# Performance work log

Hardware: AMD Instinct MI355X
Metric: run time of the kernel (lower is better)

Reference implementation:

```python
import jax, jax.numpy as jnp
import numpy as np

N, E, IN_DIM, HID, OUT = 50000, 800000, 128, 128, 64


def setup_inputs() -> dict:
    key = jax.random.key(0)
    k = jax.random.split(key, 6)
    h = jax.random.normal(k[0], (N, IN_DIM), dtype=jnp.float32)
    edge_index = jax.random.randint(k[1], (2, E), 0, N, dtype=jnp.int64)
    s_in, s_hid = 1.0 / np.sqrt(IN_DIM), 1.0 / np.sqrt(HID)
    W_gcn = jax.random.uniform(k[2], (IN_DIM, HID), jnp.float32, -s_in, s_in)
    b_gcn = jnp.zeros((HID,), jnp.float32)
    W_fc = jax.random.uniform(k[3], (HID, OUT), jnp.float32, -s_hid, s_hid)
    b_fc = jax.random.uniform(k[4], (OUT,), jnp.float32, -s_hid, s_hid)
    return {"h": h, "edge_index": edge_index, "W_gcn": W_gcn,
            "b_gcn": b_gcn, "W_fc": W_fc, "b_fc": b_fc}


def reference(h, edge_index, W_gcn, b_gcn, W_fc, b_fc):
    n = h.shape[0]
    # GCNConv: transform, add self-loops, symmetric normalization, scatter-add
    x = h @ W_gcn                                   # [N, HID]
    loop = jnp.arange(n, dtype=edge_index.dtype)
    row = jnp.concatenate([edge_index[0], loop])    # source nodes
    col = jnp.concatenate([edge_index[1], loop])    # destination nodes
    deg = jax.ops.segment_sum(jnp.ones_like(col, dtype=x.dtype), col,
                              num_segments=n)       # in-degree incl. self-loop
    dinv = jnp.where(deg > 0, jax.lax.rsqrt(deg), 0.0)
    norm = dinv[row] * dinv[col]                    # [E+N]
    msg = x[row] * norm[:, None]                    # gather + scale
    agg = jax.ops.segment_sum(msg, col, num_segments=n) + b_gcn
    # ReLU then projection
    return jax.nn.relu(agg) @ W_fc + b_fc
```

## Files before the change

kernel.cpp:

```cpp
#include <hip/hip_runtime.h>

#define N_NODES 50000
#define N_EDGES 800000
#define NBKT 782
#define BINB 196
#define BCAP 1792
#define UTS 136

typedef __attribute__((ext_vector_type(4))) float floatx4;
typedef __attribute__((ext_vector_type(8))) _Float16 half8;
typedef __attribute__((ext_vector_type(4))) _Float16 half4;
typedef __attribute__((ext_vector_type(2))) _Float16 half2v;

#define O_GF    0UL
#define O_W1    3200UL
#define O_W2    35968UL
#define O_STG   52480UL
#define O_H16   5657856UL

__global__ __launch_bounds__(256) void k_bin(const int* __restrict__ ei,
                                             int* __restrict__ gfill,
                                             unsigned* __restrict__ staging,
                                             const float* __restrict__ Wg,
                                             const float* __restrict__ Wf,
                                             _Float16* __restrict__ W1,
                                             _Float16* __restrict__ W2) {
    int b = blockIdx.x, t = threadIdx.x;
    if (b >= BINB) {
        int wb = b - BINB;
        if (wb < 64) {
            int i = wb * 256 + t;
            int n = i >> 7, k = i & 127;
            W1[i] = (_Float16)Wg[k * 128 + n];
        } else {
            int i = (wb - 64) * 256 + t;
            int n = i >> 7, k = i & 127;
            W2[i] = (_Float16)Wf[k * 64 + n];
        }
        return;
    }
    __shared__ int cnt[NBKT];
    __shared__ int gbase[NBKT];
    __shared__ int s_i64;
    if (t < 64) {
        unsigned w = ((const unsigned*)ei)[2 * t + 1];
        unsigned long long m = __ballot(w == 0u);
        if (t == 0) s_i64 = (__popcll(m) >= 60) ? 1 : 0;
    }
    for (int i = t; i < NBKT; i += 256) cnt[i] = 0;
    __syncthreads();
    bool i64 = s_i64 != 0;
    int e0 = b * 4096 + t * 16;
    int sv[16], dvv[16];
    if (i64) {
        const int4* ps = (const int4*)(ei) + (e0 >> 1);
        const int4* pd = (const int4*)(ei + 2 * (size_t)N_EDGES) + (e0 >> 1);
#pragma unroll
        for (int g = 0; g < 8; ++g) {
            if (e0 + 2 * g < N_EDGES) {
                int4 s4 = ps[g], d4 = pd[g];
                sv[2 * g] = s4.x; sv[2 * g + 1] = s4.z;
                dvv[2 * g] = d4.x; dvv[2 * g + 1] = d4.z;
            } else { dvv[2 * g] = -1; dvv[2 * g + 1] = -1; }
        }
    } else {
        const int4* ps = (const int4*)(ei) + (e0 >> 2);
        const int4* pd = (const int4*)(ei + (size_t)N_EDGES) + (e0 >> 2);
#pragma unroll
        for (int g = 0; g < 4; ++g) {
            if (e0 + 4 * g < N_EDGES) {
                int4 s4 = ps[g], d4 = pd[g];
                sv[4 * g] = s4.x; sv[4 * g + 1] = s4.y; sv[4 * g + 2] = s4.z; sv[4 * g + 3] = s4.w;
                dvv[4 * g] = d4.x; dvv[4 * g + 1] = d4.y; dvv[4 * g + 2] = d4.z; dvv[4 * g + 3] = d4.w;
            } else { dvv[4 * g] = -1; dvv[4 * g + 1] = -1; dvv[4 * g + 2] = -1; dvv[4 * g + 3] = -1; }
        }
    }
    unsigned pk[16]; int rk[16]; short bk[16];
#pragma unroll
    for (int j = 0; j < 16; ++j) {
        int d = dvv[j];
        if (d >= 0 && e0 + j < N_EDGES) {
            int bkt = d >> 6;
            bk[j] = (short)bkt;
            pk[j] = (unsigned)sv[j] | ((unsigned)(d & 63) << 16);
            rk[j] = atomicAdd(&cnt[bkt], 1);
        } else bk[j] = -1;
    }
    __syncthreads();
    for (int i = t; i < NBKT; i += 256)
        gbase[i] = atomicAdd(&gfill[i], cnt[i]);
    __syncthreads();
#pragma unroll
    for (int j = 0; j < 16; ++j) {
        if (bk[j] >= 0) {
            int pos = gbase[bk[j]] + rk[j];
            if (pos < BCAP) staging[(size_t)bk[j] * BCAP + pos] = pk[j];
        }
    }
}

__global__ __launch_bounds__(256) void k_conv(const float* __restrict__ h,
                                              const int* __restrict__ gfill,
                                              const unsigned* __restrict__ staging,
                                              _Float16* __restrict__ h16) {
    __shared__ int deg[128];
    __shared__ float sdv[128];
    int b = blockIdx.x, t = threadIdx.x;
    int nb = b * 128;
    int nn = min(128, N_NODES - nb);
    if (nn <= 0) return;
    if (t < 128) deg[t] = 0;
    __syncthreads();
#pragma unroll
    for (int kb = 0; kb < 2; ++kb) {
        int gb = b * 2 + kb;
        int cnt = min(gfill[gb], BCAP);
        const unsigned* st = staging + (size_t)gb * BCAP;
        for (int i = t; i < cnt; i += 256)
            atomicAdd(&deg[kb * 64 + (st[i] >> 16)], 1);
    }
    __syncthreads();
    if (t < 128) sdv[t] = rsqrtf((float)(deg[t] + 1));
    __syncthreads();
    const floatx4* src = (const floatx4*)(h + (size_t)nb * 128);
    half4* dst = (half4*)(h16 + (size_t)nb * 128);
    int nq = nn * 32;
    for (int i = t; i < nq; i += 256) {
        floatx4 v = src[i];
        float s = sdv[i >> 5];
        half4 o;
        o[0] = (_Float16)(v[0] * s); o[1] = (_Float16)(v[1] * s);
        o[2] = (_Float16)(v[2] * s); o[3] = (_Float16)(v[3] * s);
        dst[i] = o;
    }
}

__global__ __launch_bounds__(256, 8) void k_aggF(const _Float16* __restrict__ h16,
                                                 const int* __restrict__ gfill,
                                                 const unsigned* __restrict__ staging,
                                                 const _Float16* __restrict__ W1,
                                                 const _Float16* __restrict__ W2,
                                                 const float* __restrict__ bg,
                                                 const float* __restrict__ bfc,
                                                 float* __restrict__ out) {
    __shared__ _Float16 ut[16 * UTS];
    __shared__ _Float16 z[16 * UTS];
    __shared__ unsigned short se[BCAP];
    __shared__ int deg16[16], seg16[16], cur16[16];
    __shared__ float sdv16[16];
    int t = threadIdx.x;
    int wave = t >> 6;
    int lane = t & 63;
    int nb = blockIdx.x * 16;
    int bkt = blockIdx.x >> 2;
    unsigned lo = (unsigned)(blockIdx.x & 3) * 16;
    int cnt = min(gfill[bkt], BCAP);
    if (t < 16) deg16[t] = 0;
    __syncthreads();
    const unsigned* st = staging + (size_t)bkt * BCAP;
    unsigned held[7];
#pragma unroll
    for (int r = 0; r < 7; ++r) {
        int i = t + r * 256;
        unsigned p = 0xFFFFFFFFu;
        if (i < cnt) p = st[i];
        unsigned tg = p >> 16;
        if (tg - lo < 16u) atomicAdd(&deg16[tg - lo], 1);
        else p = 0xFFFFFFFFu;
        held[r] = p;
    }
    __syncthreads();
    if (t == 0) {
        int s = 0;
#pragma unroll
        for (int k = 0; k < 16; ++k) { seg16[k] = s; cur16[k] = s; s += deg16[k]; }
    }
    if (t < 16) sdv16[t] = rsqrtf((float)(deg16[t] + 1));
    __syncthreads();
#pragma unroll
    for (int r = 0; r < 7; ++r) {
        unsigned p = held[r];
        if (p != 0xFFFFFFFFu) {
            int rk = atomicAdd(&cur16[(p >> 16) - lo], 1);
            if (rk < BCAP) se[rk] = (unsigned short)(p & 0xffffu);
        }
    }
    __syncthreads();
    for (int q = 0; q < 4; ++q) {
        int tag = wave * 4 + q;
        int node = nb + tag;
        int p0 = seg16[tag];
        int p1 = p0 + deg16[tag];
        half2v us = *(const half2v*)(h16 + (size_t)node * 128 + lane * 2);
        float a0 = (float)us[0], a1 = (float)us[1];
        for (int base = p0; base < p1; base += 64) {
            int c = p1 - base; if (c > 64) c = 64;
            int idx = 0;
            if (lane < c) idx = se[base + lane];
            int j = 0;
            for (; j + 8 <= c; j += 8) {
                int s0 = __shfl(idx, j),     s1 = __shfl(idx, j + 1);
                int s2 = __shfl(idx, j + 2), s3 = __shfl(idx, j + 3);
                int s4 = __shfl(idx, j + 4), s5 = __shfl(idx, j + 5);
                int s6 = __shfl(idx, j + 6), s7 = __shfl(idx, j + 7);
                half2v u0 = *(const half2v*)(h16 + (size_t)s0 * 128 + lane * 2);
                half2v u1 = *(const half2v*)(h16 + (size_t)s1 * 128 + lane * 2);
                half2v u2 = *(const half2v*)(h16 + (size_t)s2 * 128 + lane * 2);
                half2v u3 = *(const half2v*)(h16 + (size_t)s3 * 128 + lane * 2);
                half2v u4 = *(const half2v*)(h16 + (size_t)s4 * 128 + lane * 2);
                half2v u5 = *(const half2v*)(h16 + (size_t)s5 * 128 + lane * 2);
                half2v u6 = *(const half2v*)(h16 + (size_t)s6 * 128 + lane * 2);
                half2v u7 = *(const half2v*)(h16 + (size_t)s7 * 128 + lane * 2);
                a0 += (float)u0[0] + (float)u1[0] + (float)u2[0] + (float)u3[0]
                    + (float)u4[0] + (float)u5[0] + (float)u6[0] + (float)u7[0];
                a1 += (float)u0[1] + (float)u1[1] + (float)u2[1] + (float)u3[1]
                    + (float)u4[1] + (float)u5[1] + (float)u6[1] + (float)u7[1];
            }
            for (; j + 4 <= c; j += 4) {
                int s0 = __shfl(idx, j),     s1 = __shfl(idx, j + 1);
                int s2 = __shfl(idx, j + 2), s3 = __shfl(idx, j + 3);
                half2v u0 = *(const half2v*)(h16 + (size_t)s0 * 128 + lane * 2);
                half2v u1 = *(const half2v*)(h16 + (size_t)s1 * 128 + lane * 2);
                half2v u2 = *(const half2v*)(h16 + (size_t)s2 * 128 + lane * 2);
                half2v u3 = *(const half2v*)(h16 + (size_t)s3 * 128 + lane * 2);
                a0 += (float)u0[0] + (float)u1[0] + (float)u2[0] + (float)u3[0];
                a1 += (float)u0[1] + (float)u1[1] + (float)u2[1] + (float)u3[1];
            }
            for (; j < c; ++j) {
                int s = __shfl(idx, j);
                half2v uu = *(const half2v*)(h16 + (size_t)s * 128 + lane * 2);
                a0 += (float)uu[0]; a1 += (float)uu[1];
            }
        }
        float sc = sdv16[tag];
        int r = wave * 4 + q;
        ut[r * UTS + lane * 2]     = (_Float16)(a0 * sc);
        ut[r * UTS + lane * 2 + 1] = (_Float16)(a1 * sc);
    }
    __syncthreads();
    int quad = lane >> 4, l15 = lane & 15;
    half8 a[4];
#pragma unroll
    for (int kk = 0; kk < 4; ++kk)
        a[kk] = *(const half8*)(ut + l15 * UTS + kk * 32 + quad * 8);
#pragma unroll
    for (int tt = 0; tt < 2; ++tt) {
        floatx4 acc = {0.f, 0.f, 0.f, 0.f};
        int n = (wave * 2 + tt) * 16 + l15;
#pragma unroll
        for (int kk = 0; kk < 4; ++kk) {
            half8 bb = *(const half8*)(W1 + n * 128 + kk * 32 + quad * 8);
            acc = __builtin_amdgcn_mfma_f32_16x16x32_f16(a[kk], bb, acc, 0, 0, 0);
        }
        float bias = bg[n];
#pragma unroll
        for (int i = 0; i < 4; ++i)
            z[(quad * 4 + i) * UTS + n] = (_Float16)fmaxf(acc[i] + bias, 0.f);
    }
    __syncthreads();
    half8 a2[4];
#pragma unroll
    for (int kk = 0; kk < 4; ++kk)
        a2[kk] = *(const half8*)(z + l15 * UTS + kk * 32 + quad * 8);
    {
        floatx4 acc = {0.f, 0.f, 0.f, 0.f};
        int n = wave * 16 + l15;
#pragma unroll
        for (int kk = 0; kk < 4; ++kk) {
            half8 bb = *(const half8*)(W2 + n * 128 + kk * 32 + quad * 8);
            acc = __builtin_amdgcn_mfma_f32_16x16x32_f16(a2[kk], bb, acc, 0, 0, 0);
        }
        float bias = bfc[n];
#pragma unroll
        for (int i = 0; i < 4; ++i)
            out[(size_t)(nb + quad * 4 + i) * 64 + n] = acc[i] + bias;
    }
}

extern "C" void kernel_launch(void* const* d_in, const int* in_sizes, int n_in,
                              void* d_out, int out_size, void* d_ws, size_t ws_size,
                              hipStream_t stream) {
    (void)in_sizes; (void)n_in; (void)out_size; (void)ws_size;
    const float* h  = (const float*)d_in[0];
    const int*   ei = (const int*)d_in[1];
    const float* Wg = (const float*)d_in[2];
    const float* bg = (const float*)d_in[3];
    const float* Wf = (const float*)d_in[4];
    const float* bf = (const float*)d_in[5];
    float* out = (float*)d_out;

    char* ws = (char*)d_ws;
    int*      gfill = (int*)(ws + O_GF);
    _Float16* W1    = (_Float16*)(ws + O_W1);
    _Float16* W2    = (_Float16*)(ws + O_W2);
    unsigned* staging = (unsigned*)(ws + O_STG);
    _Float16* h16   = (_Float16*)(ws + O_H16);

    hipMemsetAsync(gfill, 0, NBKT * sizeof(int), stream);
    k_bin<<<BINB + 96, 256, 0, stream>>>(ei, gfill, staging, Wg, Wf, W1, W2);
    k_conv<<<(N_NODES + 127) / 128, 256, 0, stream>>>(h, gfill, staging, h16);
    k_aggF<<<N_NODES / 16, 256, 0, stream>>>(h16, gfill, staging,
                                             W1, W2, bg, bf, out);
}
```

Baseline: 154.1 us.

## Replace block-local binning with per-edge global atomics on padded counters

The edge-binning kernel drops its shared-memory count/prefix phase and instead reserves each edge's slot with a global atomicAdd on a per-bucket counter. Each counter is padded to 64 bytes to avoid false sharing. Blocks now handle 1024 edges instead of 4096, giving more, lighter blocks and removing two block barriers. The cost is roughly 800k global atomics instead of a few per bucket per block, so contention on hot buckets may raise binning cost. Workspace offsets and the memset size grow to fit the padded counters.

```diff
diff --git a/kernel.cpp b/kernel.cpp
--- a/kernel.cpp
+++ b/kernel.cpp
@@ -3,7 +3,7 @@
 #define N_NODES 50000
 #define N_EDGES 800000
 #define NBKT 782
-#define BINB 196
+#define BINB 782
 #define BCAP 1792
 #define UTS 136
 
@@ -13,10 +13,10 @@
 typedef __attribute__((ext_vector_type(2))) _Float16 half2v;
 
 #define O_GF    0UL
-#define O_W1    3200UL
-#define O_W2    35968UL
-#define O_STG   52480UL
-#define O_H16   5657856UL
+#define O_W1    50048UL
+#define O_W2    82816UL
+#define O_STG   99200UL
+#define O_H16   5704576UL
 
 __global__ __launch_bounds__(256) void k_bin(const int* __restrict__ ei,
                                              int* __restrict__ gfill,
@@ -39,24 +39,21 @@
         }
         return;
     }
-    __shared__ int cnt[NBKT];
-    __shared__ int gbase[NBKT];
     __shared__ int s_i64;
     if (t < 64) {
         unsigned w = ((const unsigned*)ei)[2 * t + 1];
         unsigned long long m = __ballot(w == 0u);
         if (t == 0) s_i64 = (__popcll(m) >= 60) ? 1 : 0;
     }
-    for (int i = t; i < NBKT; i += 256) cnt[i] = 0;
     __syncthreads();
     bool i64 = s_i64 != 0;
-    int e0 = b * 4096 + t * 16;
-    int sv[16], dvv[16];
+    int e0 = b * 1024 + t * 4;
+    int sv[4], dvv[4];
     if (i64) {
         const int4* ps = (const int4*)(ei) + (e0 >> 1);
         const int4* pd = (const int4*)(ei + 2 * (size_t)N_EDGES) + (e0 >> 1);
 #pragma unroll
-        for (int g = 0; g < 8; ++g) {
+        for (int g = 0; g < 2; ++g) {
             if (e0 + 2 * g < N_EDGES) {
                 int4 s4 = ps[g], d4 = pd[g];
                 sv[2 * g] = s4.x; sv[2 * g + 1] = s4.z;
@@ -64,37 +61,21 @@
             } else { dvv[2 * g] = -1; dvv[2 * g + 1] = -1; }
         }
     } else {
-        const int4* ps = (const int4*)(ei) + (e0 >> 2);
-        const int4* pd = (const int4*)(ei + (size_t)N_EDGES) + (e0 >> 2);
-#pragma unroll
-        for (int g = 0; g < 4; ++g) {
-            if (e0 + 4 * g < N_EDGES) {
-                int4 s4 = ps[g], d4 = pd[g];
-                sv[4 * g] = s4.x; sv[4 * g + 1] = s4.y; sv[4 * g + 2] = s4.z; sv[4 * g + 3] = s4.w;
-                dvv[4 * g] = d4.x; dvv[4 * g + 1] = d4.y; dvv[4 * g + 2] = d4.z; dvv[4 * g + 3] = d4.w;
-            } else { dvv[4 * g] = -1; dvv[4 * g + 1] = -1; dvv[4 * g + 2] = -1; dvv[4 * g + 3] = -1; }
-        }
-    }
-    unsigned pk[16]; int rk[16]; short bk[16];
-#pragma unroll
-    for (int j = 0; j < 16; ++j) {
+        if (e0 < N_EDGES) {
+            int4 s4 = ((const int4*)(ei))[e0 >> 2];
+            int4 d4 = ((const int4*)(ei + (size_t)N_EDGES))[e0 >> 2];
+            sv[0] = s4.x; sv[1] = s4.y; sv[2] = s4.z; sv[3] = s4.w;
+            dvv[0] = d4.x; dvv[1] = d4.y; dvv[2] = d4.z; dvv[3] = d4.w;
+        } else { dvv[0] = -1; dvv[1] = -1; dvv[2] = -1; dvv[3] = -1; }
+    }
+#pragma unroll
+    for (int j = 0; j < 4; ++j) {
         int d = dvv[j];
         if (d >= 0 && e0 + j < N_EDGES) {
             int bkt = d >> 6;
-            bk[j] = (short)bkt;
-            pk[j] = (unsigned)sv[j] | ((unsigned)(d & 63) << 16);
-            rk[j] = atomicAdd(&cnt[bkt], 1);
-        } else bk[j] = -1;
-    }
-    __syncthreads();
-    for (int i = t; i < NBKT; i += 256)
-        gbase[i] = atomicAdd(&gfill[i], cnt[i]);
-    __syncthreads();
-#pragma unroll
-    for (int j = 0; j < 16; ++j) {
-        if (bk[j] >= 0) {
-            int pos = gbase[bk[j]] + rk[j];
-            if (pos < BCAP) staging[(size_t)bk[j] * BCAP + pos] = pk[j];
+            unsigned pk = (unsigned)sv[j] | ((unsigned)(d & 63) << 16);
+            int pos = atomicAdd(&gfill[bkt * 16], 1);
+            if (pos < BCAP) staging[(size_t)bkt * BCAP + pos] = pk;
         }
     }
 }
@@ -114,7 +95,7 @@
 #pragma unroll
     for (int kb = 0; kb < 2; ++kb) {
         int gb = b * 2 + kb;
-        int cnt = min(gfill[gb], BCAP);
+        int cnt = min(gfill[gb * 16], BCAP);
         const unsigned* st = staging + (size_t)gb * BCAP;
         for (int i = t; i < cnt; i += 256)
             atomicAdd(&deg[kb * 64 + (st[i] >> 16)], 1);
@@ -154,7 +135,7 @@
     int nb = blockIdx.x * 16;
     int bkt = blockIdx.x >> 2;
     unsigned lo = (unsigned)(blockIdx.x & 3) * 16;
-    int cnt = min(gfill[bkt], BCAP);
+    int cnt = min(gfill[bkt * 16], BCAP);
     if (t < 16) deg16[t] = 0;
     __syncthreads();
     const unsigned* st = staging + (size_t)bkt * BCAP;
@@ -296,7 +277,7 @@
     unsigned* staging = (unsigned*)(ws + O_STG);
     _Float16* h16   = (_Float16*)(ws + O_H16);
 
-    hipMemsetAsync(gfill, 0, NBKT * sizeof(int), stream);
+    hipMemsetAsync(gfill, 0, NBKT * 16 * sizeof(int), stream);
     k_bin<<<BINB + 96, 256, 0, stream>>>(ei, gfill, staging, Wg, Wf, W1, W2);
     k_conv<<<(N_NODES + 127) / 128, 256, 0, stream>>>(h, gfill, staging, h16);
     k_aggF<<<N_NODES / 16, 256, 0, stream>>>(h16, gfill, staging,
```

Measured after the change: 187.4 us. 21.7% more time.

## Move fp16 cast of h into binning kernel and apply source normalization per edge

Applied to the files above, without the earlier changes.

The fp32-to-fp16 cast of node features now runs as extra blocks inside the binning kernel, so it no longer has to wait for degree counts. The middle kernel only computes in-degrees and writes them to a global array. In the aggregation kernel, each edge entry stores the source degree alongside its index, and the per-source rsqrt weight is applied with an FMA during the gather. This shortens the pass that sits between binning and aggregation, at the cost of a scattered deg_g lookup per edge, wider shared-memory entries, and extra shuffles and rsqrt work in the inner loop.

```diff
diff --git a/kernel.cpp b/kernel.cpp
--- a/kernel.cpp
+++ b/kernel.cpp
@@ -4,6 +4,7 @@
 #define N_EDGES 800000
 #define NBKT 782
 #define BINB 196
+#define CASTB 391
 #define BCAP 1792
 #define UTS 136
 
@@ -13,19 +14,39 @@
 typedef __attribute__((ext_vector_type(2))) _Float16 half2v;
 
 #define O_GF    0UL
-#define O_W1    3200UL
-#define O_W2    35968UL
-#define O_STG   52480UL
-#define O_H16   5657856UL
+#define O_DEG   3200UL
+#define O_W1    203264UL
+#define O_W2    236032UL
+#define O_STG   252416UL
+#define O_H16   5857792UL
 
 __global__ __launch_bounds__(256) void k_bin(const int* __restrict__ ei,
+                                             const float* __restrict__ h,
                                              int* __restrict__ gfill,
                                              unsigned* __restrict__ staging,
                                              const float* __restrict__ Wg,
                                              const float* __restrict__ Wf,
                                              _Float16* __restrict__ W1,
-                                             _Float16* __restrict__ W2) {
+                                             _Float16* __restrict__ W2,
+                                             _Float16* __restrict__ h16) {
     int b = blockIdx.x, t = threadIdx.x;
+    if (b >= BINB + 96) {
+        int wb = b - (BINB + 96);
+        int nb = wb * 128;
+        int nn = min(128, N_NODES - nb);
+        if (nn <= 0) return;
+        const floatx4* src = (const floatx4*)(h + (size_t)nb * 128);
+        half4* dst = (half4*)(h16 + (size_t)nb * 128);
+        int nq = nn * 32;
+        for (int i = t; i < nq; i += 256) {
+            floatx4 v = src[i];
+            half4 o;
+            o[0] = (_Float16)v[0]; o[1] = (_Float16)v[1];
+            o[2] = (_Float16)v[2]; o[3] = (_Float16)v[3];
+            dst[i] = o;
+        }
+        return;
+    }
     if (b >= BINB) {
         int wb = b - BINB;
         if (wb < 64) {
@@ -99,12 +120,10 @@
     }
 }
 
-__global__ __launch_bounds__(256) void k_conv(const float* __restrict__ h,
-                                              const int* __restrict__ gfill,
-                                              const unsigned* __restrict__ staging,
-                                              _Float16* __restrict__ h16) {
+__global__ __launch_bounds__(256) void k_deg(const int* __restrict__ gfill,
+                                             const unsigned* __restrict__ staging,
+                                             int* __restrict__ deg_g) {
     __shared__ int deg[128];
-    __shared__ float sdv[128];
     int b = blockIdx.x, t = threadIdx.x;
     int nb = b * 128;
     int nn = min(128, N_NODES - nb);
@@ -120,24 +139,13 @@
             atomicAdd(&deg[kb * 64 + (st[i] >> 16)], 1);
     }
     __syncthreads();
-    if (t < 128) sdv[t] = rsqrtf((float)(deg[t] + 1));
-    __syncthreads();
-    const floatx4* src = (const floatx4*)(h + (size_t)nb * 128);
-    half4* dst = (half4*)(h16 + (size_t)nb * 128);
-    int nq = nn * 32;
-    for (int i = t; i < nq; i += 256) {
-        floatx4 v = src[i];
-        float s = sdv[i >> 5];
-        half4 o;
-        o[0] = (_Float16)(v[0] * s); o[1] = (_Float16)(v[1] * s);
-        o[2] = (_Float16)(v[2] * s); o[3] = (_Float16)(v[3] * s);
-        dst[i] = o;
-    }
+    if (t < nn) deg_g[nb + t] = deg[t];
 }
 
 __global__ __launch_bounds__(256, 8) void k_aggF(const _Float16* __restrict__ h16,
                                                  const int* __restrict__ gfill,
                                                  const unsigned* __restrict__ staging,
+                                                 const int* __restrict__ deg_g,
                                                  const _Float16* __restrict__ W1,
                                                  const _Float16* __restrict__ W2,
                                                  const float* __restrict__ bg,
@@ -145,7 +153,7 @@
                                                  float* __restrict__ out) {
     __shared__ _Float16 ut[16 * UTS];
     __shared__ _Float16 z[16 * UTS];
-    __shared__ unsigned short se[BCAP];
+    __shared__ unsigned se32[BCAP];
     __shared__ int deg16[16], seg16[16], cur16[16];
     __shared__ float sdv16[16];
     int t = threadIdx.x;
@@ -158,15 +166,18 @@
     if (t < 16) deg16[t] = 0;
     __syncthreads();
     const unsigned* st = staging + (size_t)bkt * BCAP;
-    unsigned held[7];
+    unsigned held[7]; int dgv[7];
 #pragma unroll
     for (int r = 0; r < 7; ++r) {
         int i = t + r * 256;
         unsigned p = 0xFFFFFFFFu;
         if (i < cnt) p = st[i];
         unsigned tg = p >> 16;
-        if (tg - lo < 16u) atomicAdd(&deg16[tg - lo], 1);
-        else p = 0xFFFFFFFFu;
+        dgv[r] = 0;
+        if (tg - lo < 16u) {
+            atomicAdd(&deg16[tg - lo], 1);
+            dgv[r] = deg_g[p & 0xFFFFu];
+        } else p = 0xFFFFFFFFu;
         held[r] = p;
     }
     __syncthreads();
@@ -182,7 +193,7 @@
         unsigned p = held[r];
         if (p != 0xFFFFFFFFu) {
             int rk = atomicAdd(&cur16[(p >> 16) - lo], 1);
-            if (rk < BCAP) se[rk] = (unsigned short)(p & 0xffffu);
+            if (rk < BCAP) se32[rk] = ((unsigned)dgv[r] << 16) | (p & 0xFFFFu);
         }
     }
     __syncthreads();
@@ -191,48 +202,62 @@
         int node = nb + tag;
         int p0 = seg16[tag];
         int p1 = p0 + deg16[tag];
+        float sc = sdv16[tag];
         half2v us = *(const half2v*)(h16 + (size_t)node * 128 + lane * 2);
-        float a0 = (float)us[0], a1 = (float)us[1];
+        float a0 = (float)us[0] * sc, a1 = (float)us[1] * sc;
         for (int base = p0; base < p1; base += 64) {
             int c = p1 - base; if (c > 64) c = 64;
             int idx = 0;
-            if (lane < c) idx = se[base + lane];
+            if (lane < c) idx = (int)se32[base + lane];
+            float wf = rsqrtf((float)((unsigned)idx >> 16) + 1.f);
             int j = 0;
             for (; j + 8 <= c; j += 8) {
                 int s0 = __shfl(idx, j),     s1 = __shfl(idx, j + 1);
                 int s2 = __shfl(idx, j + 2), s3 = __shfl(idx, j + 3);
                 int s4 = __shfl(idx, j + 4), s5 = __shfl(idx, j + 5);
                 int s6 = __shfl(idx, j + 6), s7 = __shfl(idx, j + 7);
-                half2v u0 = *(const half2v*)(h16 + (size_t)s0 * 128 + lane * 2);
-                half2v u1 = *(const half2v*)(h16 + (size_t)s1 * 128 + lane * 2);
-                half2v u2 = *(const half2v*)(h16 + (size_t)s2 * 128 + lane * 2);
-                half2v u3 = *(const half2v*)(h16 + (size_t)s3 * 128 + lane * 2);
-                half2v u4 = *(const half2v*)(h16 + (size_t)s4 * 128 + lane * 2);
-                half2v u5 = *(const half2v*)(h16 + (size_t)s5 * 128 + lane * 2);
-                half2v u6 = *(const half2v*)(h16 + (size_t)s6 * 128 + lane * 2);
-                half2v u7 = *(const half2v*)(h16 + (size_t)s7 * 128 + lane * 2);
-                a0 += (float)u0[0] + (float)u1[0] + (float)u2[0] + (float)u3[0]
-                    + (float)u4[0] + (float)u5[0] + (float)u6[0] + (float)u7[0];
-                a1 += (float)u0[1] + (float)u1[1] + (float)u2[1] + (float)u3[1]
-                    + (float)u4[1] + (float)u5[1] + (float)u6[1] + (float)u7[1];
+                float f0 = __shfl(wf, j),     f1 = __shfl(wf, j + 1);
+                float f2 = __shfl(wf, j + 2), f3 = __shfl(wf, j + 3);
+                float f4 = __shfl(wf, j + 4), f5 = __shfl(wf, j + 5);
+                float f6 = __shfl(wf, j + 6), f7 = __shfl(wf, j + 7);
+                half2v u0 = *(const half2v*)(h16 + (size_t)(s0 & 0xFFFF) * 128 + lane * 2);
+                half2v u1 = *(const half2v*)(h16 + (size_t)(s1 & 0xFFFF) * 128 + lane * 2);
+                half2v u2 = *(const half2v*)(h16 + (size_t)(s2 & 0xFFFF) * 128 + lane * 2);
+                half2v u3 = *(const half2v*)(h16 + (size_t)(s3 & 0xFFFF) * 128 + lane * 2);
+                half2v u4 = *(const half2v*)(h16 + (size_t)(s4 & 0xFFFF) * 128 + lane * 2);
+                half2v u5 = *(const half2v*)(h16 + (size_t)(s5 & 0xFFFF) * 128 + lane * 2);
+                half2v u6 = *(const half2v*)(h16 + (size_t)(s6 & 0xFFFF) * 128 + lane * 2);
+                half2v u7 = *(const half2v*)(h16 + (size_t)(s7 & 0xFFFF) * 128 + lane * 2);
+                a0 = fmaf((float)u0[0], f0, a0); a1 = fmaf((float)u0[1], f0, a1);
+                a0 = fmaf((float)u1[0], f1, a0); a1 = fmaf((float)u1[1], f1, a1);
+                a0 = fmaf((float)u2[0], f2, a0); a1 = fmaf((float)u2[1], f2, a1);
+                a0 = fmaf((float)u3[0], f3, a0); a1 = fmaf((float)u3[1], f3, a1);
+                a0 = fmaf((float)u4[0], f4, a0); a1 = fmaf((float)u4[1], f4, a1);
+                a0 = fmaf((float)u5[0], f5, a0); a1 = fmaf((float)u5[1], f5, a1);
+                a0 = fmaf((float)u6[0], f6, a0); a1 = fmaf((float)u6[1], f6, a1);
+                a0 = fmaf((float)u7[0], f7, a0); a1 = fmaf((float)u7[1], f7, a1);
             }
             for (; j + 4 <= c; j += 4) {
                 int s0 = __shfl(idx, j),     s1 = __shfl(idx, j + 1);
                 int s2 = __shfl(idx, j + 2), s3 = __shfl(idx, j + 3);
-                half2v u0 = *(const half2v*)(h16 + (size_t)s0 * 128 + lane * 2);
-                half2v u1 = *(const half2v*)(h16 + (size_t)s1 * 128 + lane * 2);
-                half2v u2 = *(const half2v*)(h16 + (size_t)s2 * 128 + lane * 2);
-                half2v u3 = *(const half2v*)(h16 + (size_t)s3 * 128 + lane * 2);
-                a0 += (float)u0[0] + (float)u1[0] + (float)u2[0] + (float)u3[0];
-                a1 += (float)u0[1] + (float)u1[1] + (float)u2[1] + (float)u3[1];
+                float f0 = __shfl(wf, j),     f1 = __shfl(wf, j + 1);
+                float f2 = __shfl(wf, j + 2), f3 = __shfl(wf, j + 3);
+                half2v u0 = *(const half2v*)(h16 + (size_t)(s0 & 0xFFFF) * 128 + lane * 2);
+                half2v u1 = *(const half2v*)(h16 + (size_t)(s1 & 0xFFFF) * 128 + lane * 2);
+                half2v u2 = *(const half2v*)(h16 + (size_t)(s2 & 0xFFFF) * 128 + lane * 2);
+                half2v u3 = *(const half2v*)(h16 + (size_t)(s3 & 0xFFFF) * 128 + lane * 2);
+                a0 = fmaf((float)u0[0], f0, a0); a1 = fmaf((float)u0[1], f0, a1);
+                a0 = fmaf((float)u1[0], f1, a0); a1 = fmaf((float)u1[1], f1, a1);
+                a0 = fmaf((float)u2[0], f2, a0); a1 = fmaf((float)u2[1], f2, a1);
+                a0 = fmaf((float)u3[0], f3, a0); a1 = fmaf((float)u3[1], f3, a1);
             }
             for (; j < c; ++j) {
                 int s = __shfl(idx, j);
-                half2v uu = *(const half2v*)(h16 + (size_t)s * 128 + lane * 2);
-                a0 += (float)uu[0]; a1 += (float)uu[1];
+                float f = __shfl(wf, j);
+                half2v uu = *(const half2v*)(h16 + (size_t)(s & 0xFFFF) * 128 + lane * 2);
+                a0 = fmaf((float)uu[0], f, a0); a1 = fmaf((float)uu[1], f, a1);
             }
         }
-        float sc = sdv16[tag];
         int r = wave * 4 + q;
         ut[r * UTS + lane * 2]     = (_Float16)(a0 * sc);
         ut[r * UTS + lane * 2 + 1] = (_Float16)(a1 * sc);
@@ -291,14 +316,16 @@
 
     char* ws = (char*)d_ws;
     int*      gfill = (int*)(ws + O_GF);
+    int*      deg_g = (int*)(ws + O_DEG);
     _Float16* W1    = (_Float16*)(ws + O_W1);
     _Float16* W2    = (_Float16*)(ws + O_W2);
     unsigned* staging = (unsigned*)(ws + O_STG);
     _Float16* h16   = (_Float16*)(ws + O_H16);
 
     hipMemsetAsync(gfill, 0, NBKT * sizeof(int), stream);
-    k_bin<<<BINB + 96, 256, 0, stream>>>(ei, gfill, staging, Wg, Wf, W1, W2);
-    k_conv<<<(N_NODES + 127) / 128, 256, 0, stream>>>(h, gfill, staging, h16);
-    k_aggF<<<N_NODES / 16, 256, 0, stream>>>(h16, gfill, staging,
+    k_bin<<<BINB + 96 + CASTB, 256, 0, stream>>>(ei, h, gfill, staging,
+                                                 Wg, Wf, W1, W2, h16);
+    k_deg<<<(N_NODES + 127) / 128, 256, 0, stream>>>(gfill, staging, deg_g);
+    k_aggF<<<N_NODES / 16, 256, 0, stream>>>(h16, gfill, staging, deg_g,
                                              W1, W2, bg, bf, out);
 }
```

Measured after the change: 151.6 us. No clear change (-1.6%).
